# Performance work log

Measured on AMD Instinct MI355X. Metric: run time of the kernel, lower is better.

The kernel has to match this reference:

```python
import jax, jax.numpy as jnp
import numpy as np

NUM_HEADS = 8
HEAD_DIM = 64


def setup_inputs() -> dict:
    key = jax.random.key(0)
    k0, k1, k2, k3 = jax.random.split(key, 4)
    B, S, Dm = 16, 4096, 512
    x = jax.random.normal(k0, (B, S, Dm), dtype=jnp.float32)
    W_q = jax.random.normal(k1, (Dm, NUM_HEADS * HEAD_DIM), dtype=jnp.float32) * 0.02
    W_k = jax.random.normal(k2, (Dm, NUM_HEADS * HEAD_DIM), dtype=jnp.float32) * 0.02
    W_v = jax.random.normal(k3, (Dm, NUM_HEADS * HEAD_DIM), dtype=jnp.float32) * 0.02
    return {"x": x, "W_q": W_q, "W_k": W_k, "W_v": W_v}


def reference(x, W_q, W_k, W_v):
    B, S, _ = x.shape
    H, D = NUM_HEADS, HEAD_DIM
    # projections -> (B, S, H, D); NOTE: original keeps layout (B,S,H,D)
    # without transposing, so tf.matmul batches over (B,S): attention is
    # computed ACROSS HEADS per token (HxH scores), unscaled. Faithful here.
    q = (x @ W_q).reshape(B, S, H, D)
    k = (x @ W_k).reshape(B, S, H, D)
    v = (x @ W_v).reshape(B, S, H, D)
    scores = jnp.einsum("bshd,bstd->bsht", q, k)  # (B,S,H,H)
    attn = jax.nn.softmax(scores, axis=-1)
    out = jnp.einsum("bsht,bstd->bshd", attn, v)  # (B,S,H,D)
    return out.reshape(B, S, H * D)
```

## Files before the change

kernel.cpp:

```cpp
#include <hip/hip_runtime.h>
#include <hip/hip_bf16.h>

typedef __bf16 bf16_t;
typedef __bf16 bf16x8 __attribute__((ext_vector_type(8)));
typedef float  f32x4  __attribute__((ext_vector_type(4)));

#define DM    512
#define NQKV  1536
#define NTOK  65536
#define TM    32
#define QSTR  1544

__device__ __align__(16) bf16_t g_wt2[(size_t)NQKV * DM];

#define MEMFENCE asm volatile("" ::: "memory")

__global__ void prep_w2(const float* __restrict__ Wq,
                        const float* __restrict__ Wk,
                        const float* __restrict__ Wv) {
    int flat = blockIdx.x * 256 + threadIdx.x;
    int l  = flat & 63;
    int kg = l >> 4, lr = l & 15;
    int t2 = flat >> 6;
    int ni = t2 % 12;
    int t3 = t2 / 12;
    int s  = t3 & 15, w = t3 >> 4;
    int n  = w * 192 + ni * 16 + lr;
    int k0 = s * 32 + kg * 8;
    int mat = n >> 9, nn = n & 511;
    const float* W = (mat == 0) ? Wq : ((mat == 1) ? Wk : Wv);
    bf16x8 v;
#pragma unroll
    for (int e = 0; e < 8; ++e) v[e] = (bf16_t)W[(k0 + e) * DM + nn];
    *(bf16x8*)(g_wt2 + (size_t)flat * 8) = v;
}

__global__ __launch_bounds__(512, 1) void fused_mha(
    const float* __restrict__ x, float* __restrict__ out) {
    extern __shared__ char sm[];

    const int tid = threadIdx.x;
    const int l   = tid & 63, w = tid >> 6;
    const int lr  = l & 15,  kg = l >> 4;
    const size_t tok0 = (size_t)blockIdx.x * TM;

    {
        const int r = tid >> 4, tj = tid & 15, r7 = r & 7;
        const float* xp = x + (tok0 + r) * DM;
#pragma unroll
        for (int j = 0; j < 4; ++j) {
            int c = tj + j * 16;
            float4 f0 = *(const float4*)(xp + c * 8);
            float4 f1 = *(const float4*)(xp + c * 8 + 4);
            bf16x8 v;
            v[0] = (bf16_t)f0.x; v[1] = (bf16_t)f0.y;
            v[2] = (bf16_t)f0.z; v[3] = (bf16_t)f0.w;
            v[4] = (bf16_t)f1.x; v[5] = (bf16_t)f1.y;
            v[6] = (bf16_t)f1.z; v[7] = (bf16_t)f1.w;
            *(bf16x8*)(sm + r * 1024 + ((c ^ r7) << 4)) = v;
        }
    }

    const bf16_t* gw = g_wt2 + ((size_t)w * 16 * 12 * 64 + l) * 8;
    bf16x8 H0[6], H1[6], H2[6], H3[6], H4[6];

#define LOADH(H, h_)                                                          \
    _Pragma("unroll")                                                         \
    for (int ni = 0; ni < 6; ++ni)                                            \
        H[ni] = *(const bf16x8*)(gw + (h_) * 3072 + ni * 512);

    LOADH(H0, 0) LOADH(H1, 1) LOADH(H2, 2) LOADH(H3, 3) LOADH(H4, 4)

    asm volatile("s_waitcnt lgkmcnt(0)" ::: "memory");
    __builtin_amdgcn_s_barrier();
    MEMFENCE;

    f32x4 acc[2][12];
#pragma unroll
    for (int a = 0; a < 2; ++a)
#pragma unroll
        for (int b = 0; b < 12; ++b) acc[a][b] = (f32x4){0.f, 0.f, 0.f, 0.f};

    const int sx = (lr & 7) << 4;
    bf16x8 af[2];

#define HALF(h_, H) do {                                                      \
        if (((h_) & 1) == 0) {                                                \
            af[0] = *(const bf16x8*)(sm + lr * 1024 +                         \
                                     ((((h_) >> 1) * 64 + kg * 16) ^ sx));    \
            af[1] = *(const bf16x8*)(sm + 16384 + lr * 1024 +                 \
                                     ((((h_) >> 1) * 64 + kg * 16) ^ sx));    \
        }                                                                     \
        _Pragma("unroll")                                                     \
        for (int mi = 0; mi < 2; ++mi)                                        \
        _Pragma("unroll")                                                     \
        for (int ni = 0; ni < 6; ++ni)                                        \
            acc[mi][((h_) & 1) * 6 + ni] =                                    \
                __builtin_amdgcn_mfma_f32_16x16x32_bf16(                      \
                    af[mi], H[ni], acc[mi][((h_) & 1) * 6 + ni], 0, 0, 0);    \
        if ((h_) + 5 < 32) { LOADH(H, (h_) + 5) }                             \
    } while (0)

    HALF( 0, H0); HALF( 1, H1); HALF( 2, H2); HALF( 3, H3); HALF( 4, H4);
    HALF( 5, H0); HALF( 6, H1); HALF( 7, H2); HALF( 8, H3); HALF( 9, H4);
    HALF(10, H0); HALF(11, H1); HALF(12, H2); HALF(13, H3); HALF(14, H4);
    HALF(15, H0); HALF(16, H1); HALF(17, H2); HALF(18, H3); HALF(19, H4);
    HALF(20, H0); HALF(21, H1); HALF(22, H2); HALF(23, H3); HALF(24, H4);
    HALF(25, H0); HALF(26, H1); HALF(27, H2); HALF(28, H3); HALF(29, H4);
    HALF(30, H0); HALF(31, H1);
#undef HALF
#undef LOADH

    asm volatile("s_waitcnt lgkmcnt(0)" ::: "memory");
    __builtin_amdgcn_s_barrier();
    MEMFENCE;

    bf16_t* qkv = (bf16_t*)sm;
#pragma unroll
    for (int mi = 0; mi < 2; ++mi)
#pragma unroll
        for (int ni = 0; ni < 12; ++ni) {
            int col = w * 192 + ni * 16 + lr;
#pragma unroll
            for (int i = 0; i < 4; ++i) {
                int token = mi * 16 + kg * 4 + i;
                qkv[token * QSTR + col] = (bf16_t)acc[mi][ni][i];
            }
        }
    asm volatile("s_waitcnt lgkmcnt(0)" ::: "memory");
    __builtin_amdgcn_s_barrier();
    MEMFENCE;

    const int tok = tid >> 4, tj = tid & 15, h = tj & 7, d0 = (tj >> 3) << 5;
    const bf16_t* base = qkv + tok * QSTR;

    float qv[32];
    {
        const bf16_t* qp = base + h * 64 + d0;
#pragma unroll
        for (int j = 0; j < 4; ++j) {
            bf16x8 q8 = *(const bf16x8*)(qp + 8 * j);
#pragma unroll
            for (int e = 0; e < 8; ++e) qv[8 * j + e] = (float)q8[e];
        }
    }

    float s[8];
#pragma unroll
    for (int t = 0; t < 8; ++t) {
        const bf16_t* kp = base + 512 + t * 64 + d0;
        float a = 0.f;
#pragma unroll
        for (int j = 0; j < 4; ++j) {
            bf16x8 k8 = *(const bf16x8*)(kp + 8 * j);
#pragma unroll
            for (int e = 0; e < 8; ++e) a += qv[8 * j + e] * (float)k8[e];
        }
        s[t] = a;
    }
#pragma unroll
    for (int t = 0; t < 8; ++t) s[t] += __shfl_xor(s[t], 8, 64);

    float m = s[0];
#pragma unroll
    for (int t = 1; t < 8; ++t) m = fmaxf(m, s[t]);
    float p[8], psum = 0.f;
#pragma unroll
    for (int t = 0; t < 8; ++t) {
        p[t] = exp2f((s[t] - m) * 1.44269504088896f);
        psum += p[t];
    }
    float inv = 1.0f / psum;

    float o[32];
#pragma unroll
    for (int e = 0; e < 32; ++e) o[e] = 0.f;
#pragma unroll
    for (int t = 0; t < 8; ++t) {
        float pt = p[t] * inv;
        const bf16_t* vp = base + 1024 + t * 64 + d0;
#pragma unroll
        for (int j = 0; j < 4; ++j) {
            bf16x8 v8 = *(const bf16x8*)(vp + 8 * j);
#pragma unroll
            for (int e = 0; e < 8; ++e) o[8 * j + e] += pt * (float)v8[e];
        }
    }

    float* op = out + (tok0 + tok) * DM + h * 64 + d0;
#pragma unroll
    for (int j = 0; j < 8; ++j) {
        float4 o4 = {o[4 * j], o[4 * j + 1], o[4 * j + 2], o[4 * j + 3]};
        *(float4*)(op + 4 * j) = o4;
    }
}

extern "C" void kernel_launch(void* const* d_in, const int* in_sizes, int n_in,
                              void* d_out, int out_size, void* d_ws, size_t ws_size,
                              hipStream_t stream) {
    (void)d_ws; (void)ws_size; (void)n_in; (void)out_size;
    const float* x  = (const float*)d_in[0];
    const float* Wq = (const float*)d_in[1];
    const float* Wk = (const float*)d_in[2];
    const float* Wv = (const float*)d_in[3];
    float* out = (float*)d_out;

    int ntok = in_sizes[0] / DM;
    prep_w2<<<384, 256, 0, stream>>>(Wq, Wk, Wv);
    size_t lds = (size_t)TM * QSTR * sizeof(bf16_t);
    fused_mha<<<ntok / TM, 512, lds, stream>>>(x, out);
}
```

Before: 244.4 us.

## Stream weight tiles into a per-wave LDS double buffer via global_load_lds

Replaces the five-deep register prefetch of weight fragments with a per-wave, two-slot LDS ring filled by asynchronous global-to-LDS loads. Each step waits on vmcnt, reads the fragments from LDS, issues the load two steps ahead, and raises wave priority around the MFMA block. The aim is to cut VGPR pressure and let weight fetches overlap compute without occupying registers. In exchange, prefetch depth drops from five steps to two, every fragment pays an extra LDS read, and the dynamic LDS allocation grows to 128 KB.

```diff
diff --git a/kernel.cpp b/kernel.cpp
--- a/kernel.cpp
+++ b/kernel.cpp
@@ -14,6 +14,12 @@
 __device__ __align__(16) bf16_t g_wt2[(size_t)NQKV * DM];
 
 #define MEMFENCE asm volatile("" ::: "memory")
+
+typedef const void __attribute__((address_space(1)))* gas_t;
+typedef void       __attribute__((address_space(3)))* sas_t;
+__device__ __forceinline__ void gl_lds16(const void* g, void* s) {
+    __builtin_amdgcn_global_load_lds((gas_t)g, (sas_t)s, 16, 0, 0);
+}
 
 __global__ void prep_w2(const float* __restrict__ Wq,
                         const float* __restrict__ Wk,
@@ -61,16 +67,19 @@
         }
     }
 
-    const bf16_t* gw = g_wt2 + ((size_t)w * 16 * 12 * 64 + l) * 8;
-    bf16x8 H0[6], H1[6], H2[6], H3[6], H4[6];
-
-#define LOADH(H, h_)                                                          \
-    _Pragma("unroll")                                                         \
-    for (int ni = 0; ni < 6; ++ni)                                            \
-        H[ni] = *(const bf16x8*)(gw + (h_) * 3072 + ni * 512);
-
-    LOADH(H0, 0) LOADH(H1, 1) LOADH(H2, 2) LOADH(H3, 3) LOADH(H4, 4)
-
+    const bf16_t* gwB = g_wt2 + (size_t)w * 98304 + l * 8;
+    char* ringW = sm + 32768 + w * 12288;
+
+#define ISSUE6(h_)                                                            \
+    do {                                                                      \
+        _Pragma("unroll")                                                     \
+        for (int ii = 0; ii < 6; ++ii)                                        \
+            gl_lds16(gwB + (size_t)(h_) * 3072 + ii * 512,                    \
+                     ringW + ((h_) & 1) * 6144 + ii * 1024);                  \
+    } while (0)
+#define WAITVM(n_) asm volatile("s_waitcnt vmcnt(" #n_ ")" ::: "memory")
+
+    ISSUE6(0); ISSUE6(1);
     asm volatile("s_waitcnt lgkmcnt(0)" ::: "memory");
     __builtin_amdgcn_s_barrier();
     MEMFENCE;
@@ -84,34 +93,47 @@
     const int sx = (lr & 7) << 4;
     bf16x8 af[2];
 
-#define HALF(h_, H) do {                                                      \
+#define HSTEP(h_, vm_)                                                        \
+    do {                                                                      \
+        WAITVM(vm_);                     \
+        bf16x8 bf_[6];                                                        \
+        _Pragma("unroll")                                                     \
+        for (int ni = 0; ni < 6; ++ni)                                        \
+            bf_[ni] = *(const bf16x8*)(ringW + ((h_) & 1) * 6144 +            \
+                                       ni * 1024 + l * 16);                   \
         if (((h_) & 1) == 0) {                                                \
             af[0] = *(const bf16x8*)(sm + lr * 1024 +                         \
                                      ((((h_) >> 1) * 64 + kg * 16) ^ sx));    \
             af[1] = *(const bf16x8*)(sm + 16384 + lr * 1024 +                 \
                                      ((((h_) >> 1) * 64 + kg * 16) ^ sx));    \
         }                                                                     \
+        asm volatile("s_waitcnt lgkmcnt(0)" ::: "memory");                    \
+        __builtin_amdgcn_sched_barrier(0);                      \
+        if ((h_) + 2 < 32) ISSUE6((h_) + 2);           \
+        __builtin_amdgcn_s_setprio(1);                                        \
         _Pragma("unroll")                                                     \
         for (int mi = 0; mi < 2; ++mi)                                        \
         _Pragma("unroll")                                                     \
         for (int ni = 0; ni < 6; ++ni)                                        \
             acc[mi][((h_) & 1) * 6 + ni] =                                    \
                 __builtin_amdgcn_mfma_f32_16x16x32_bf16(                      \
-                    af[mi], H[ni], acc[mi][((h_) & 1) * 6 + ni], 0, 0, 0);    \
-        if ((h_) + 5 < 32) { LOADH(H, (h_) + 5) }                             \
+                    af[mi], bf_[ni], acc[mi][((h_) & 1) * 6 + ni], 0, 0, 0);  \
+        __builtin_amdgcn_s_setprio(0);                                        \
     } while (0)
 
-    HALF( 0, H0); HALF( 1, H1); HALF( 2, H2); HALF( 3, H3); HALF( 4, H4);
-    HALF( 5, H0); HALF( 6, H1); HALF( 7, H2); HALF( 8, H3); HALF( 9, H4);
-    HALF(10, H0); HALF(11, H1); HALF(12, H2); HALF(13, H3); HALF(14, H4);
-    HALF(15, H0); HALF(16, H1); HALF(17, H2); HALF(18, H3); HALF(19, H4);
-    HALF(20, H0); HALF(21, H1); HALF(22, H2); HALF(23, H3); HALF(24, H4);
-    HALF(25, H0); HALF(26, H1); HALF(27, H2); HALF(28, H3); HALF(29, H4);
-    HALF(30, H0); HALF(31, H1);
-#undef HALF
-#undef LOADH
-
-    asm volatile("s_waitcnt lgkmcnt(0)" ::: "memory");
+    HSTEP( 0, 6); HSTEP( 1, 6); HSTEP( 2, 6); HSTEP( 3, 6);
+    HSTEP( 4, 6); HSTEP( 5, 6); HSTEP( 6, 6); HSTEP( 7, 6);
+    HSTEP( 8, 6); HSTEP( 9, 6); HSTEP(10, 6); HSTEP(11, 6);
+    HSTEP(12, 6); HSTEP(13, 6); HSTEP(14, 6); HSTEP(15, 6);
+    HSTEP(16, 6); HSTEP(17, 6); HSTEP(18, 6); HSTEP(19, 6);
+    HSTEP(20, 6); HSTEP(21, 6); HSTEP(22, 6); HSTEP(23, 6);
+    HSTEP(24, 6); HSTEP(25, 6); HSTEP(26, 6); HSTEP(27, 6);
+    HSTEP(28, 6); HSTEP(29, 6); HSTEP(30, 6); HSTEP(31, 0);
+#undef HSTEP
+#undef ISSUE6
+#undef WAITVM
+
+    asm volatile("s_waitcnt vmcnt(0) lgkmcnt(0)" ::: "memory");
     __builtin_amdgcn_s_barrier();
     MEMFENCE;
 
@@ -207,6 +229,6 @@
 
     int ntok = in_sizes[0] / DM;
     prep_w2<<<384, 256, 0, stream>>>(Wq, Wk, Wv);
-    size_t lds = (size_t)TM * QSTR * sizeof(bf16_t);
+    size_t lds = 131072;
     fused_mha<<<ntok / TM, 512, lds, stream>>>(x, out);
 }
```

New measurement: 214.6 us. -12.2%, faster.
